# Kernel tuning notes

Hardware: AMD Instinct MI355X
Metric: run time of the kernel (lower is better)

## Reference

```python
import jax, jax.numpy as jnp
import numpy as np

HIDDEN = 128
MIN_DIST = 0.01


def setup_inputs() -> dict:
    key = jax.random.key(0)
    ks = jax.random.split(key, 7)
    B, N, D = 4, 1024, 3
    pos_scaled = jax.random.normal(ks[0], (B, N, D), dtype=jnp.float32)
    # PyTorch Linear: y = x @ W.T + b ; store W as (in, out) for clean einsum
    s1 = 1.0 / np.sqrt(3.0)
    s2 = 1.0 / np.sqrt(HIDDEN)
    W1 = jax.random.uniform(ks[1], (3, HIDDEN), jnp.float32, -s1, s1)
    b1 = jax.random.uniform(ks[2], (HIDDEN,), jnp.float32, -s1, s1)
    W2 = jax.random.uniform(ks[3], (HIDDEN, HIDDEN), jnp.float32, -s2, s2)
    b2 = jax.random.uniform(ks[4], (HIDDEN,), jnp.float32, -s2, s2)
    W3 = jax.random.uniform(ks[5], (HIDDEN, 1), jnp.float32, -s2, s2)
    b3 = jax.random.uniform(ks[6], (1,), jnp.float32, -s2, s2)
    return {"pos_scaled": pos_scaled, "W1": W1, "b1": b1, "W2": W2, "b2": b2, "W3": W3, "b3": b3}


def reference(pos_scaled, W1, b1, W2, b2, W3, b3):
    B, N, _ = pos_scaled.shape
    diff = pos_scaled[:, :, None, :] - pos_scaled[:, None, :, :]   # (B,N,N,3)
    dist = jnp.linalg.norm(diff, axis=-1, keepdims=True)           # (B,N,N,1)
    dist_clip = jnp.maximum(dist, MIN_DIST)
    inv_r = 1.0 / dist_clip
    feat = jnp.concatenate([dist, inv_r, inv_r * inv_r], axis=-1)  # (B,N,N,3)
    h = jnp.tanh(feat @ W1 + b1)
    h = jnp.tanh(h @ W2 + b2)
    mag = h @ W3 + b3                                              # (B,N,N,1)
    mask = (~jnp.eye(N, dtype=bool))[None, :, :, None]             # (1,N,N,1)
    pair_forces = jnp.where(mask, mag * (diff / dist_clip), 0.0)
    return jnp.sum(pair_forces, axis=2)                            # (B,N,3)
```

## Files before the change

### kernel.cpp

```cpp
#include <hip/hip_runtime.h>

#define NPTS  1024
#define HID   128
#define K_TAB 4096
#define U0f   (-10.0f)
#define U1f   (4.0f)

__device__ __forceinline__ float fast_exp2(float x) {
#if __has_builtin(__builtin_amdgcn_exp2f)
    return __builtin_amdgcn_exp2f(x);
#else
    return exp2f(x);
#endif
}
__device__ __forceinline__ float fast_rcp(float x) {
#if __has_builtin(__builtin_amdgcn_rcpf)
    return __builtin_amdgcn_rcpf(x);
#else
    return 1.0f / x;
#endif
}
__device__ __forceinline__ float fast_log2(float x) {
#if __has_builtin(__builtin_amdgcn_logf)
    return __builtin_amdgcn_logf(x);
#else
    return __log2f(x);
#endif
}
__device__ __forceinline__ float fast_rsq(float x) {
#if __has_builtin(__builtin_amdgcn_rsqf)
    return __builtin_amdgcn_rsqf(x);
#else
    return rsqrtf(x);
#endif
}
__device__ __forceinline__ float fast_tanh(float x) {
    float e = fast_exp2(2.8853900817779268f * x);
    return 1.0f - 2.0f * fast_rcp(e + 1.0f);
}

__global__ __launch_bounds__(256) void build_table(const float* __restrict__ W1,
                                                   const float* __restrict__ b1,
                                                   const float* __restrict__ W2,
                                                   const float* __restrict__ b2,
                                                   const float* __restrict__ W3,
                                                   const float* __restrict__ b3,
                                                   float2* __restrict__ tab)
{
    __shared__ float W2s[HID * HID];
    __shared__ float h1s[4][HID];
    __shared__ float mag_s[36];

    const int t = threadIdx.x, wave = t >> 6, lane = t & 63;

    for (int idx = t; idx < HID * HID; idx += 256) W2s[idx] = W2[idx];

    const float w10a = W1[lane],      w11a = W1[HID + lane],      w12a = W1[2 * HID + lane],      b1a = b1[lane];
    const float w10b = W1[lane + 64], w11b = W1[HID + lane + 64], w12b = W1[2 * HID + lane + 64], b1b = b1[lane + 64];
    const float2 b2l = ((const float2*)b2)[lane];
    const float2 w3l = ((const float2*)W3)[lane];
    const float  b3v = b3[0];
    const float  dU  = (U1f - U0f) / (float)(K_TAB - 1);
    const int    e0  = blockIdx.x * 32;

    __syncthreads();

    for (int r = 0; r < 9; ++r) {
        int  ei    = wave + 4 * r;
        bool valid = (ei <= 32);
        if (valid) {
            float u    = U0f + (float)(e0 + ei) * dU;
            float d    = fast_exp2(u);
            float invc = 1.0f / fmaxf(d, 0.01f);
            float inv2 = invc * invc;
            float za = fmaf(d, w10a, fmaf(invc, w11a, fmaf(inv2, w12a, b1a)));
            float zb = fmaf(d, w10b, fmaf(invc, w11b, fmaf(inv2, w12b, b1b)));
            h1s[wave][lane]      = fast_tanh(za);
            h1s[wave][lane + 64] = fast_tanh(zb);
        }
        __syncthreads();
        if (valid) {
            float a0 = b2l.x, a1 = b2l.y;
#pragma unroll 8
            for (int k = 0; k < HID; ++k) {
                float  h = h1s[wave][k];
                float2 w = ((const float2*)W2s)[k * 64 + lane];
                a0 = fmaf(h, w.x, a0);
                a1 = fmaf(h, w.y, a1);
            }
            float part = fast_tanh(a0) * w3l.x + fast_tanh(a1) * w3l.y;
#pragma unroll
            for (int off = 1; off < 64; off <<= 1) part += __shfl_xor(part, off);
            if (lane == 0) mag_s[ei] = part + b3v;
        }
        __syncthreads();
    }

    if (t < 32) {
        int e = e0 + t;
        tab[e] = make_float2(mag_s[t], mag_s[t + 1] - mag_s[t]);
    }
}

__global__ __launch_bounds__(256) void forces_kernel(const float* __restrict__ pos,
                                                     const float2* __restrict__ tab,
                                                     float* __restrict__ out)
{
    __shared__ float2 tab_s[K_TAB];
    __shared__ float  pos_s[NPTS * 3];

    const int t = threadIdx.x, wave = t >> 6, lane = t & 63;
    const int b  = blockIdx.x >> 8;
    const int ig = blockIdx.x & 255;
    const int i  = ig * 4 + wave;

    {
        const float4* gp = (const float4*)(pos + b * NPTS * 3);
        float4* sp = (float4*)pos_s;
        for (int idx = t; idx < 768; idx += 256) sp[idx] = gp[idx];
        const float4* gt = (const float4*)tab;
        float4* st = (float4*)tab_s;
        for (int idx = t; idx < 2048; idx += 256) st[idx] = gt[idx];
    }
    __syncthreads();

    const float pix = pos_s[i * 3 + 0];
    const float piy = pos_s[i * 3 + 1];
    const float piz = pos_s[i * 3 + 2];
    const float S   = (float)(K_TAB - 1) / (U1f - U0f);

    float fx = 0.f, fy = 0.f, fz = 0.f;
#pragma unroll 4
    for (int j = lane; j < NPTS; j += 64) {
        float dx = pix - pos_s[j * 3 + 0];
        float dy = piy - pos_s[j * 3 + 1];
        float dz = piz - pos_s[j * 3 + 2];
        float r2 = fmaf(dx, dx, fmaf(dy, dy, dz * dz));
        float u  = 0.5f * fast_log2(r2);
        float tt = (u - U0f) * S;
        float kf = fminf(fmaxf(floorf(tt), 0.0f), (float)(K_TAB - 2));
        float fr = fminf(fmaxf(tt - kf, 0.0f), 1.0f);
        int   k  = (int)kf;
        float2 te = tab_s[k];
        float mag  = fmaf(te.y, fr, te.x);
        float invd = fminf(fast_rsq(r2), 100.0f);
        float s = mag * invd;
        fx = fmaf(s, dx, fx);
        fy = fmaf(s, dy, fy);
        fz = fmaf(s, dz, fz);
    }
#pragma unroll
    for (int off = 1; off < 64; off <<= 1) {
        fx += __shfl_xor(fx, off);
        fy += __shfl_xor(fy, off);
        fz += __shfl_xor(fz, off);
    }
    if (lane == 0) {
        int o = (b * NPTS + i) * 3;
        out[o + 0] = fx;
        out[o + 1] = fy;
        out[o + 2] = fz;
    }
}

extern "C" void kernel_launch(void* const* d_in, const int* in_sizes, int n_in,
                              void* d_out, int out_size, void* d_ws, size_t ws_size,
                              hipStream_t stream) {
    const float* pos = (const float*)d_in[0];
    const float* W1  = (const float*)d_in[1];
    const float* b1  = (const float*)d_in[2];
    const float* W2  = (const float*)d_in[3];
    const float* b2  = (const float*)d_in[4];
    const float* W3  = (const float*)d_in[5];
    const float* b3  = (const float*)d_in[6];
    float* out = (float*)d_out;

    float2* tab = (float2*)d_ws;

    int B = (in_sizes[0] / 3) / NPTS;
    build_table<<<K_TAB / 32, 256, 0, stream>>>(W1, b1, W2, b2, W3, b3, tab);
    forces_kernel<<<B * 256, 256, 0, stream>>>(pos, tab, out);
}
```

Before: 93.28 us.

## Fuse table build and force pass into one cooperative kernel with grid sync

Merges the MLP lookup-table construction and the pairwise force accumulation into a single cooperative launch separated by a grid-wide sync, removing one kernel launch. The table build now processes 8 entries per block iteration, reading W2 directly from global memory instead of staging it in LDS, and stores scalar table values with neighbor lookup instead of (value, delta) pairs. The force pass halves the grid, with each wave handling two target points so position loads are shared. This adds grid-sync cost and cooperative launch constraints, and changes how the table is sampled.

```diff
diff --git a/kernel.cpp b/kernel.cpp
--- a/kernel.cpp
+++ b/kernel.cpp
@@ -1,10 +1,14 @@
 #include <hip/hip_runtime.h>
-
-#define NPTS  1024
-#define HID   128
-#define K_TAB 4096
-#define U0f   (-10.0f)
-#define U1f   (4.0f)
+#include <hip/hip_cooperative_groups.h>
+
+namespace cg = cooperative_groups;
+
+#define NPTS   1024
+#define HID    128
+#define K_TAB  4096
+#define U0f    (-10.0f)
+#define U1f    (4.0f)
+#define GPB    128
 
 __device__ __forceinline__ float fast_exp2(float x) {
 #if __has_builtin(__builtin_amdgcn_exp2f)
@@ -39,127 +43,147 @@
     return 1.0f - 2.0f * fast_rcp(e + 1.0f);
 }
 
-__global__ __launch_bounds__(256) void build_table(const float* __restrict__ W1,
-                                                   const float* __restrict__ b1,
-                                                   const float* __restrict__ W2,
-                                                   const float* __restrict__ b2,
-                                                   const float* __restrict__ W3,
-                                                   const float* __restrict__ b3,
-                                                   float2* __restrict__ tab)
+__global__ __launch_bounds__(256, 2)
+void discovery_fused(const float* __restrict__ pos,
+                     const float* __restrict__ W1,
+                     const float* __restrict__ b1,
+                     const float* __restrict__ W2,
+                     const float* __restrict__ b2,
+                     const float* __restrict__ W3,
+                     const float* __restrict__ b3,
+                     float* __restrict__ tabg,
+                     float* __restrict__ out)
 {
-    __shared__ float W2s[HID * HID];
-    __shared__ float h1s[4][HID];
-    __shared__ float mag_s[36];
-
-    const int t = threadIdx.x, wave = t >> 6, lane = t & 63;
-
-    for (int idx = t; idx < HID * HID; idx += 256) W2s[idx] = W2[idx];
-
-    const float w10a = W1[lane],      w11a = W1[HID + lane],      w12a = W1[2 * HID + lane],      b1a = b1[lane];
-    const float w10b = W1[lane + 64], w11b = W1[HID + lane + 64], w12b = W1[2 * HID + lane + 64], b1b = b1[lane + 64];
-    const float2 b2l = ((const float2*)b2)[lane];
-    const float2 w3l = ((const float2*)W3)[lane];
-    const float  b3v = b3[0];
-    const float  dU  = (U1f - U0f) / (float)(K_TAB - 1);
-    const int    e0  = blockIdx.x * 32;
-
-    __syncthreads();
-
-    for (int r = 0; r < 9; ++r) {
-        int  ei    = wave + 4 * r;
-        bool valid = (ei <= 32);
-        if (valid) {
-            float u    = U0f + (float)(e0 + ei) * dU;
+    __shared__ __align__(16) char smem[(K_TAB + 4) * 4 + NPTS * 3 * 4];
+    float (*h1s)[HID] = (float (*)[HID])smem;
+    float (*red)[HID] = (float (*)[HID])(smem + 8 * HID * 4);
+    float* tab_s = (float*)smem;
+    float* pos_s = (float*)(smem + (K_TAB + 4) * 4);
+
+    const int t    = threadIdx.x;
+    const int wave = t >> 6;
+    const int lane = t & 63;
+    const float dU  = (U1f - U0f) / (float)K_TAB;
+    const float b3v = b3[0];
+
+    for (int e0 = blockIdx.x * 8; e0 < K_TAB; e0 += gridDim.x * 8) {
+        for (int tau = t; tau < 8 * HID; tau += 256) {
+            int ee = tau >> 7, n = tau & 127;
+            float u    = U0f + (float)(e0 + ee) * dU;
             float d    = fast_exp2(u);
-            float invc = 1.0f / fmaxf(d, 0.01f);
+            float invc = fast_rcp(fmaxf(d, 0.01f));
             float inv2 = invc * invc;
-            float za = fmaf(d, w10a, fmaf(invc, w11a, fmaf(inv2, w12a, b1a)));
-            float zb = fmaf(d, w10b, fmaf(invc, w11b, fmaf(inv2, w12b, b1b)));
-            h1s[wave][lane]      = fast_tanh(za);
-            h1s[wave][lane + 64] = fast_tanh(zb);
-        }
-        __syncthreads();
-        if (valid) {
-            float a0 = b2l.x, a1 = b2l.y;
+            float z = fmaf(d, W1[n], fmaf(invc, W1[HID + n], fmaf(inv2, W1[2 * HID + n], b1[n])));
+            h1s[ee][n] = fast_tanh(z);
+        }
+        __syncthreads();
+        {
+            int n = t & 127, eh = (t >> 7) * 4;
+            float a0 = b2[n], a1 = a0, a2 = a0, a3 = a0;
 #pragma unroll 8
             for (int k = 0; k < HID; ++k) {
-                float  h = h1s[wave][k];
-                float2 w = ((const float2*)W2s)[k * 64 + lane];
-                a0 = fmaf(h, w.x, a0);
-                a1 = fmaf(h, w.y, a1);
+                float w = W2[k * HID + n];
+                a0 = fmaf(h1s[eh + 0][k], w, a0);
+                a1 = fmaf(h1s[eh + 1][k], w, a1);
+                a2 = fmaf(h1s[eh + 2][k], w, a2);
+                a3 = fmaf(h1s[eh + 3][k], w, a3);
             }
-            float part = fast_tanh(a0) * w3l.x + fast_tanh(a1) * w3l.y;
+            float w3n = W3[n];
+            red[eh + 0][n] = fast_tanh(a0) * w3n;
+            red[eh + 1][n] = fast_tanh(a1) * w3n;
+            red[eh + 2][n] = fast_tanh(a2) * w3n;
+            red[eh + 3][n] = fast_tanh(a3) * w3n;
+        }
+        __syncthreads();
+        for (int ee = wave; ee < 8; ee += 4) {
+            float s = red[ee][lane] + red[ee][lane + 64];
 #pragma unroll
-            for (int off = 1; off < 64; off <<= 1) part += __shfl_xor(part, off);
-            if (lane == 0) mag_s[ei] = part + b3v;
-        }
-        __syncthreads();
-    }
-
-    if (t < 32) {
-        int e = e0 + t;
-        tab[e] = make_float2(mag_s[t], mag_s[t + 1] - mag_s[t]);
-    }
-}
-
-__global__ __launch_bounds__(256) void forces_kernel(const float* __restrict__ pos,
-                                                     const float2* __restrict__ tab,
-                                                     float* __restrict__ out)
-{
-    __shared__ float2 tab_s[K_TAB];
-    __shared__ float  pos_s[NPTS * 3];
-
-    const int t = threadIdx.x, wave = t >> 6, lane = t & 63;
-    const int b  = blockIdx.x >> 8;
-    const int ig = blockIdx.x & 255;
-    const int i  = ig * 4 + wave;
-
+            for (int off = 1; off < 64; off <<= 1) s += __shfl_xor(s, off);
+            if (lane == 0) tabg[e0 + ee] = s + b3v;
+        }
+        __syncthreads();
+    }
+    if (blockIdx.x == 0) {
+        float d    = fast_exp2(U1f);
+        float invc = fast_rcp(fmaxf(d, 0.01f));
+        float inv2 = invc * invc;
+        if (t < HID) {
+            float z = fmaf(d, W1[t], fmaf(invc, W1[HID + t], fmaf(inv2, W1[2 * HID + t], b1[t])));
+            h1s[0][t] = fast_tanh(z);
+        }
+        __syncthreads();
+        if (t < HID) {
+            float a = b2[t];
+#pragma unroll 8
+            for (int k = 0; k < HID; ++k) a = fmaf(h1s[0][k], W2[k * HID + t], a);
+            red[0][t] = fast_tanh(a) * W3[t];
+        }
+        __syncthreads();
+        if (wave == 0) {
+            float s = red[0][lane] + red[0][lane + 64];
+#pragma unroll
+            for (int off = 1; off < 64; off <<= 1) s += __shfl_xor(s, off);
+            if (lane == 0) tabg[K_TAB] = s + b3v;
+        }
+    }
+
+    cg::this_grid().sync();
+
+    const int b  = blockIdx.x / GPB;
+    const int ig = blockIdx.x % GPB;
+
+    for (int idx = t; idx <= K_TAB; idx += 256) tab_s[idx] = tabg[idx];
     {
         const float4* gp = (const float4*)(pos + b * NPTS * 3);
         float4* sp = (float4*)pos_s;
-        for (int idx = t; idx < 768; idx += 256) sp[idx] = gp[idx];
-        const float4* gt = (const float4*)tab;
-        float4* st = (float4*)tab_s;
-        for (int idx = t; idx < 2048; idx += 256) st[idx] = gt[idx];
+        for (int idx = t; idx < NPTS * 3 / 4; idx += 256) sp[idx] = gp[idx];
     }
     __syncthreads();
 
-    const float pix = pos_s[i * 3 + 0];
-    const float piy = pos_s[i * 3 + 1];
-    const float piz = pos_s[i * 3 + 2];
-    const float S   = (float)(K_TAB - 1) / (U1f - U0f);
-
-    float fx = 0.f, fy = 0.f, fz = 0.f;
+    const int   ia = ig * 8 + wave;
+    const int   ib = ia + 4;
+    const float pax = pos_s[ia * 3 + 0], pay = pos_s[ia * 3 + 1], paz = pos_s[ia * 3 + 2];
+    const float pbx = pos_s[ib * 3 + 0], pby = pos_s[ib * 3 + 1], pbz = pos_s[ib * 3 + 2];
+    const float S = (float)K_TAB / (U1f - U0f);
+
+    float fax = 0.f, fay = 0.f, faz = 0.f;
+    float fbx = 0.f, fby = 0.f, fbz = 0.f;
 #pragma unroll 4
     for (int j = lane; j < NPTS; j += 64) {
-        float dx = pix - pos_s[j * 3 + 0];
-        float dy = piy - pos_s[j * 3 + 1];
-        float dz = piz - pos_s[j * 3 + 2];
-        float r2 = fmaf(dx, dx, fmaf(dy, dy, dz * dz));
-        float u  = 0.5f * fast_log2(r2);
-        float tt = (u - U0f) * S;
-        float kf = fminf(fmaxf(floorf(tt), 0.0f), (float)(K_TAB - 2));
-        float fr = fminf(fmaxf(tt - kf, 0.0f), 1.0f);
-        int   k  = (int)kf;
-        float2 te = tab_s[k];
-        float mag  = fmaf(te.y, fr, te.x);
-        float invd = fminf(fast_rsq(r2), 100.0f);
-        float s = mag * invd;
-        fx = fmaf(s, dx, fx);
-        fy = fmaf(s, dy, fy);
-        fz = fmaf(s, dz, fz);
+        float qx = pos_s[j * 3 + 0], qy = pos_s[j * 3 + 1], qz = pos_s[j * 3 + 2];
+
+        float dax = pax - qx, day = pay - qy, daz = paz - qz;
+        float dbx = pbx - qx, dby = pby - qy, dbz = pbz - qz;
+        float r2a = fmaf(dax, dax, fmaf(day, day, daz * daz));
+        float r2b = fmaf(dbx, dbx, fmaf(dby, dby, dbz * dbz));
+
+        float ta = fmaf(0.5f * fast_log2(r2a), S, -U0f * S);
+        float tb = fmaf(0.5f * fast_log2(r2b), S, -U0f * S);
+        float ka = fminf(fmaxf(floorf(ta), 0.0f), (float)(K_TAB - 1));
+        float kb = fminf(fmaxf(floorf(tb), 0.0f), (float)(K_TAB - 1));
+        float fra = fminf(fmaxf(ta - ka, 0.0f), 1.0f);
+        float frb = fminf(fmaxf(tb - kb, 0.0f), 1.0f);
+        int ia4 = (int)ka, ib4 = (int)kb;
+        float va0 = tab_s[ia4], va1 = tab_s[ia4 + 1];
+        float vb0 = tab_s[ib4], vb1 = tab_s[ib4 + 1];
+        float maga = fmaf(va1 - va0, fra, va0);
+        float magb = fmaf(vb1 - vb0, frb, vb0);
+
+        float sa = maga * fminf(fast_rsq(r2a), 100.0f);
+        float sb = magb * fminf(fast_rsq(r2b), 100.0f);
+        fax = fmaf(sa, dax, fax); fay = fmaf(sa, day, fay); faz = fmaf(sa, daz, faz);
+        fbx = fmaf(sb, dbx, fbx); fby = fmaf(sb, dby, fby); fbz = fmaf(sb, dbz, fbz);
     }
 #pragma unroll
     for (int off = 1; off < 64; off <<= 1) {
-        fx += __shfl_xor(fx, off);
-        fy += __shfl_xor(fy, off);
-        fz += __shfl_xor(fz, off);
+        fax += __shfl_xor(fax, off); fay += __shfl_xor(fay, off); faz += __shfl_xor(faz, off);
+        fbx += __shfl_xor(fbx, off); fby += __shfl_xor(fby, off); fbz += __shfl_xor(fbz, off);
     }
     if (lane == 0) {
-        int o = (b * NPTS + i) * 3;
-        out[o + 0] = fx;
-        out[o + 1] = fy;
-        out[o + 2] = fz;
+        int oa = (b * NPTS + ia) * 3;
+        int ob = (b * NPTS + ib) * 3;
+        out[oa + 0] = fax; out[oa + 1] = fay; out[oa + 2] = faz;
+        out[ob + 0] = fbx; out[ob + 1] = fby; out[ob + 2] = fbz;
     }
 }
 
@@ -173,11 +197,12 @@
     const float* b2  = (const float*)d_in[4];
     const float* W3  = (const float*)d_in[5];
     const float* b3  = (const float*)d_in[6];
-    float* out = (float*)d_out;
-
-    float2* tab = (float2*)d_ws;
+    float* out  = (float*)d_out;
+    float* tabg = (float*)d_ws;
 
     int B = (in_sizes[0] / 3) / NPTS;
-    build_table<<<K_TAB / 32, 256, 0, stream>>>(W1, b1, W2, b2, W3, b3, tab);
-    forces_kernel<<<B * 256, 256, 0, stream>>>(pos, tab, out);
-}
+    dim3 grid(B * GPB), block(256);
+    void* args[] = { (void*)&pos, (void*)&W1, (void*)&b1, (void*)&W2, (void*)&b2,
+                     (void*)&W3, (void*)&b3, (void*)&tabg, (void*)&out };
+    hipLaunchCooperativeKernel((const void*)discovery_fused, grid, block, args, 0, stream);
+}
```

Result: slower. 145.2 us (+55.7%).
